# Kernel tuning notes

Measured on AMD Instinct MI355X. Metric: run time of the kernel, lower is better.

## Reference

```python
import jax, jax.numpy as jnp
import numpy as np

U, I, D, NNZ, LAYERS, B = 50000, 50000, 64, 3200000, 3, 4096
N = U + I
L2_REG = 1e-5
EPS = 1e-12


def setup_inputs() -> dict:
    key = jax.random.key(0)
    ks = jax.random.split(key, 12)
    return {
        "users": jax.random.randint(ks[0], (B,), 0, U, dtype=jnp.int64)
        if jax.config.jax_enable_x64 else jax.random.randint(ks[0], (B,), 0, U, dtype=jnp.int32),
        "pos_items": jax.random.randint(ks[1], (B,), 0, N, dtype=jnp.int32),
        "neg_items": jax.random.randint(ks[2], (B,), 0, N, dtype=jnp.int32),
        "rows": jax.random.randint(ks[3], (NNZ,), 0, N, dtype=jnp.int32),
        "cols": jax.random.randint(ks[4], (NNZ,), 0, N, dtype=jnp.int32),
        "vals": jax.random.uniform(ks[5], (NNZ,), dtype=jnp.float32),
        "user_embed": jax.random.normal(ks[6], (U, D), dtype=jnp.float32),
        "item_embed": jax.random.normal(ks[7], (I, D), dtype=jnp.float32),
        "W1": jax.random.normal(ks[8], (LAYERS, D, D), dtype=jnp.float32) * 0.1,
        "b1": jax.random.normal(ks[9], (LAYERS, 1, D), dtype=jnp.float32) * 0.1,
        "W2": jax.random.normal(ks[10], (LAYERS, D, D), dtype=jnp.float32) * 0.1,
        "b2": jax.random.normal(ks[11], (LAYERS, 1, D), dtype=jnp.float32) * 0.1,
    }


def reference(users, pos_items, neg_items, rows, cols, vals,
              user_embed, item_embed, W1, b1, W2, b2):
    # E: [N, D] concatenated user/item embeddings
    E = jnp.concatenate([user_embed, item_embed], axis=0)
    embs = [E]
    for l in range(W1.shape[0]):
        # SpMM: L @ E via edge-wise gather + scatter-add (memory-bound)
        msgs = vals[:, None] * E[cols]                     # [nnz, D]
        L_mul = jax.ops.segment_sum(msgs, rows, num_segments=N)
        A_mul = L_mul + E                                  # A = L + I
        left = A_mul @ W1[l] + b1[l]
        right = (L_mul * E) @ W2[l] + b2[l]
        E = jax.nn.leaky_relu(left + right, negative_slope=0.2)
        # message dropout rate = 0 -> identity
        norm = jnp.maximum(jnp.linalg.norm(E, axis=1, keepdims=True), EPS)
        embs.append(E / norm)
    all_e = jnp.concatenate(embs, axis=1)                  # [N, D*(LAYERS+1)]
    u = all_e[users]
    p = all_e[pos_items]
    n = all_e[neg_items]
    pos_rating = jnp.sum(u * p, axis=1)
    neg_rating = jnp.sum(u * n, axis=1)
    bpr_loss = -jnp.mean(jax.nn.log_sigmoid(pos_rating - neg_rating))
    # faithful to source: neg term is ||n|| (not squared)
    l2norm = (jnp.sum(u ** 2) + jnp.sum(p ** 2) + jnp.sqrt(jnp.sum(n ** 2))) / 2.0
    l2reg = L2_REG * l2norm / u.shape[0]
    return bpr_loss + l2reg
```

## Files before the change

kernel.cpp:

```cpp
#include <hip/hip_runtime.h>
#include <hip/hip_bf16.h>
#include <math.h>

#define U_CNT 50000
#define I_CNT 50000
#define N_CNT 100000
#define D 64
#define NNZ_CNT 3200000
#define LAYERS 3
#define BATCH 4096
#define L2_REG_F 1e-5f
#define EPS_F 1e-12f

#define NBUCKET 391
#define SC_NBLK 256
#define SC_CHUNK 12500
#define BCNT_N (NBUCKET * SC_NBLK)
#define BCNT_NBLK ((BCNT_N + 255) / 256)

typedef __attribute__((ext_vector_type(8))) short short8;
typedef __attribute__((ext_vector_type(4))) float floatx4;

__device__ __forceinline__ unsigned short f32_to_bf16(float f) {
    unsigned int u = __float_as_uint(f);
    u += 0x7FFFu + ((u >> 16) & 1u);
    return (unsigned short)(u >> 16);
}
__device__ __forceinline__ float bf16_to_f32(unsigned short h) {
    return __uint_as_float(((unsigned int)h) << 16);
}
__device__ __forceinline__ float bf16_lo(unsigned int u) {
    return __uint_as_float(u << 16);
}
__device__ __forceinline__ float bf16_hi(unsigned int u) {
    return __uint_as_float(u & 0xFFFF0000u);
}
__device__ __forceinline__ unsigned int pack_bf16(float a, float b) {
    return (unsigned int)f32_to_bf16(a) | ((unsigned int)f32_to_bf16(b) << 16);
}

__global__ void init_E(const float* __restrict__ ue, const float* __restrict__ ie,
                       unsigned short* __restrict__ Ebf, float* __restrict__ all_e) {
    int tid = blockIdx.x * blockDim.x + threadIdx.x;
    if (tid >= N_CNT * D) return;
    int row = tid >> 6;
    int d = tid & 63;
    float v = (row < U_CNT) ? ue[tid] : ie[tid - U_CNT * D];
    Ebf[tid] = f32_to_bf16(v);
    all_e[(size_t)row * 256 + d] = v;
}

__global__ void scan_p1(const int* __restrict__ in, int* __restrict__ bsums, int n) {
    __shared__ int s[256];
    int t = threadIdx.x;
    int i = blockIdx.x * 256 + t;
    int v = (i < n) ? in[i] : 0;
    s[t] = v;
    __syncthreads();
    for (int off = 128; off >= 1; off >>= 1) {
        if (t < off) s[t] += s[t + off];
        __syncthreads();
    }
    if (t == 0) bsums[blockIdx.x] = s[0];
}

__global__ void scan_p2(int* __restrict__ bsums, int nblk) {
    __shared__ int s[512];
    int t = threadIdx.x;
    int v = (t < nblk) ? bsums[t] : 0;
    s[t] = v;
    __syncthreads();
    for (int off = 1; off < 512; off <<= 1) {
        int x = (t >= off) ? s[t - off] : 0;
        __syncthreads();
        s[t] += x;
        __syncthreads();
    }
    if (t < nblk) bsums[t] = s[t] - v;
}

__global__ void scan_p3(const int* __restrict__ in, const int* __restrict__ bsums,
                        int* __restrict__ out, int n) {
    __shared__ int s[256];
    int t = threadIdx.x;
    int i = blockIdx.x * 256 + t;
    int v = (i < n) ? in[i] : 0;
    s[t] = v;
    __syncthreads();
    for (int off = 1; off < 256; off <<= 1) {
        int x = (t >= off) ? s[t - off] : 0;
        __syncthreads();
        s[t] += x;
        __syncthreads();
    }
    if (i < n) out[i] = s[t] - v + bsums[blockIdx.x];
}

__global__ __launch_bounds__(1024) void bucket_hist(const int* __restrict__ rows,
                                                    int* __restrict__ bcnt) {
    __shared__ int h[NBUCKET];
    int blk = blockIdx.x, t = threadIdx.x;
    if (t < NBUCKET) h[t] = 0;
    __syncthreads();
    int s = blk * SC_CHUNK, e = s + SC_CHUNK;
    for (int i = s + t; i < e; i += 1024) atomicAdd(&h[rows[i] >> 8], 1);
    __syncthreads();
    if (t < NBUCKET) bcnt[t * SC_NBLK + blk] = h[t];
}

__global__ __launch_bounds__(1024) void block_scatter(const int* __restrict__ rows,
                                                      const int* __restrict__ cols,
                                                      const float* __restrict__ vals,
                                                      const int* __restrict__ boff,
                                                      float2* __restrict__ bbuf) {
    __shared__ int cur[NBUCKET];
    int blk = blockIdx.x, t = threadIdx.x;
    if (t < NBUCKET) cur[t] = boff[t * SC_NBLK + blk];
    __syncthreads();
    int s = blk * SC_CHUNK, e = s + SC_CHUNK;
    for (int i = s + t; i < e; i += 1024) {
        int r = rows[i];
        int b = r >> 8;
        int p = atomicAdd(&cur[b], 1);
        unsigned int bits = ((unsigned int)(r & 255) << 17) | (unsigned int)cols[i];
        bbuf[p] = make_float2(vals[i], __uint_as_float(bits));
    }
}

__global__ __launch_bounds__(1024) void csr_finalize(const float2* __restrict__ bbuf,
                                                     const int* __restrict__ boff,
                                                     int* __restrict__ row_ptr,
                                                     float2* __restrict__ packed) {
    __shared__ int h[256];
    __shared__ int cur[256];
    int b = blockIdx.x, t = threadIdx.x;
    int s = boff[b * SC_NBLK];
    int e = (b == NBUCKET - 1) ? NNZ_CNT : boff[(b + 1) * SC_NBLK];
    if (t < 256) h[t] = 0;
    __syncthreads();
    for (int i = s + t; i < e; i += 1024)
        atomicAdd(&h[__float_as_uint(bbuf[i].y) >> 17], 1);
    __syncthreads();
    int v = (t < 256) ? h[t] : 0;
    for (int off = 1; off < 256; off <<= 1) {
        int x = (t >= off && t < 256) ? h[t - off] : 0;
        __syncthreads();
        if (t < 256) h[t] += x;
        __syncthreads();
    }
    if (t < 256) {
        int start = s + h[t] - v;
        int row = (b << 8) + t;
        if (row < N_CNT) row_ptr[row] = start;
        cur[t] = start;
        if (b == 0 && t == 0) row_ptr[N_CNT] = NNZ_CNT;
    }
    __syncthreads();
    for (int i = s + t; i < e; i += 1024) {
        float2 rec = bbuf[i];
        unsigned int bits = __float_as_uint(rec.y);
        int p = atomicAdd(&cur[bits >> 17], 1);
        packed[p] = make_float2(rec.x, __int_as_float(bits & 0x1FFFFu));
    }
}

__global__ __launch_bounds__(256) void spmm_bf16(const float2* __restrict__ packed,
                                                 const int* __restrict__ row_ptr,
                                                 const unsigned short* __restrict__ Ebf,
                                                 unsigned short* __restrict__ Lm) {
    int wid = (blockIdx.x * blockDim.x + threadIdx.x) >> 6;
    int lane = threadIdx.x & 63;
    if (wid >= N_CNT) return;
    int s = row_ptr[wid];
    int e = row_ptr[wid + 1];
    int sub = lane >> 2;
    int sl = lane & 3;
    int eidx = sub >> 1;
    int half = sub & 1;
    int dbase = half * 32 + sl * 8;
    float a0 = 0.f, a1 = 0.f, a2 = 0.f, a3 = 0.f;
    float a4 = 0.f, a5 = 0.f, a6 = 0.f, a7 = 0.f;
    int i = s + eidx;
    float2 rec = (i < e) ? packed[i] : make_float2(0.f, __int_as_float(0));
    while (i < e) {
        int inext = i + 8;
        float2 rnext = (inext < e) ? packed[inext] : make_float2(0.f, __int_as_float(0));
        int c = __float_as_int(rec.y);
        uint4 ev = *(const uint4*)(Ebf + (size_t)c * D + dbase);
        float v = rec.x;
        a0 += v * bf16_lo(ev.x); a1 += v * bf16_hi(ev.x);
        a2 += v * bf16_lo(ev.y); a3 += v * bf16_hi(ev.y);
        a4 += v * bf16_lo(ev.z); a5 += v * bf16_hi(ev.z);
        a6 += v * bf16_lo(ev.w); a7 += v * bf16_hi(ev.w);
        rec = rnext;
        i = inext;
    }
#pragma unroll
    for (int off = 32; off >= 8; off >>= 1) {
        a0 += __shfl_xor(a0, off, 64); a1 += __shfl_xor(a1, off, 64);
        a2 += __shfl_xor(a2, off, 64); a3 += __shfl_xor(a3, off, 64);
        a4 += __shfl_xor(a4, off, 64); a5 += __shfl_xor(a5, off, 64);
        a6 += __shfl_xor(a6, off, 64); a7 += __shfl_xor(a7, off, 64);
    }
    if (eidx == 0) {
        unsigned int* dst = (unsigned int*)(Lm + (size_t)wid * D + dbase);
        *(uint4*)dst = make_uint4(pack_bf16(a0, a1), pack_bf16(a2, a3),
                                  pack_bf16(a4, a5), pack_bf16(a6, a7));
    }
}

#define AP 136
__global__ __launch_bounds__(256) void layer_fused_mfma(const unsigned short* __restrict__ Lm,
                                                        unsigned short* __restrict__ Ebf,
                                                        const float* __restrict__ W1,
                                                        const float* __restrict__ b1,
                                                        const float* __restrict__ W2,
                                                        const float* __restrict__ b2,
                                                        float* __restrict__ all_e, int layer) {
    __shared__ unsigned short sBt[64 * AP];
    __shared__ float sBias[64];
    __shared__ unsigned short sA[4][16 * AP];

    int t = threadIdx.x;
    for (int i = t; i < 4096; i += 256) {
        int k = i >> 6, n = i & 63;
        sBt[n * AP + k] = f32_to_bf16(W1[i]);
        sBt[n * AP + 64 + k] = f32_to_bf16(W2[i]);
    }
    if (t < 64) sBias[t] = b1[t] + b2[t];
    __syncthreads();

    int w = t >> 6, lane = t & 63;
    int quad = lane >> 4, l16 = lane & 15;

    short8 bfrag[4][4];
#pragma unroll
    for (int ks = 0; ks < 4; ks++)
#pragma unroll
        for (int ct = 0; ct < 4; ct++)
            bfrag[ks][ct] = *(const short8*)&sBt[(ct * 16 + l16) * AP + ks * 32 + quad * 8];

    float bias[4];
#pragma unroll
    for (int ct = 0; ct < 4; ct++) bias[ct] = sBias[ct * 16 + l16];

    unsigned short* A = sA[w];
    int col_off = (layer + 1) * 64;
    int nwaves = gridDim.x * 4;

    for (int tile = blockIdx.x * 4 + w; tile < N_CNT / 16; tile += nwaves) {
        int rbase = tile * 16;
#pragma unroll
        for (int p = 0; p < 4; p++) {
            int r = p * 4 + quad;
            int c = l16 * 4;
            uint2 lw = *(const uint2*)(Lm + (size_t)(rbase + r) * 64 + c);
            float l0 = bf16_lo(lw.x), l1 = bf16_hi(lw.x);
            float l2 = bf16_lo(lw.y), l3 = bf16_hi(lw.y);
            ushort4 eh = *(const ushort4*)(Ebf + (size_t)(rbase + r) * 64 + c);
            float e0 = bf16_to_f32(eh.x), e1 = bf16_to_f32(eh.y);
            float e2 = bf16_to_f32(eh.z), e3 = bf16_to_f32(eh.w);
            *(uint2*)&A[r * AP + c] = make_uint2(pack_bf16(l0 + e0, l1 + e1),
                                                pack_bf16(l2 + e2, l3 + e3));
            *(uint2*)&A[r * AP + 64 + c] = make_uint2(pack_bf16(l0 * e0, l1 * e1),
                                                      pack_bf16(l2 * e2, l3 * e3));
        }
        floatx4 acc[4];
#pragma unroll
        for (int ct = 0; ct < 4; ct++) {
            acc[ct][0] = bias[ct]; acc[ct][1] = bias[ct];
            acc[ct][2] = bias[ct]; acc[ct][3] = bias[ct];
        }
#pragma unroll
        for (int ks = 0; ks < 4; ks++) {
            short8 af = *(const short8*)&A[l16 * AP + ks * 32 + quad * 8];
#pragma unroll
            for (int ct = 0; ct < 4; ct++)
                acc[ct] = __builtin_amdgcn_mfma_f32_16x16x32_bf16(af, bfrag[ks][ct], acc[ct], 0, 0, 0);
        }
        float y[4][4];
        float ssq[4] = {0.f, 0.f, 0.f, 0.f};
#pragma unroll
        for (int ct = 0; ct < 4; ct++)
#pragma unroll
            for (int reg = 0; reg < 4; reg++) {
                float v = acc[ct][reg];
                v = (v > 0.f) ? v : 0.2f * v;
                y[ct][reg] = v;
                ssq[reg] += v * v;
            }
#pragma unroll
        for (int reg = 0; reg < 4; reg++) {
            float ss = ssq[reg];
            ss += __shfl_xor(ss, 1, 64);
            ss += __shfl_xor(ss, 2, 64);
            ss += __shfl_xor(ss, 4, 64);
            ss += __shfl_xor(ss, 8, 64);
            ssq[reg] = fmaxf(sqrtf(ss), EPS_F);
        }
#pragma unroll
        for (int reg = 0; reg < 4; reg++) {
            int row = rbase + quad * 4 + reg;
            float inv = 1.0f / ssq[reg];
#pragma unroll
            for (int ct = 0; ct < 4; ct++) {
                int col = ct * 16 + l16;
                float v = y[ct][reg];
                Ebf[(size_t)row * 64 + col] = f32_to_bf16(v);
                all_e[(size_t)row * 256 + col_off + col] = v * inv;
            }
        }
    }
}

__device__ __forceinline__ float dot4(float4 a, float4 b) {
    return a.x * b.x + a.y * b.y + a.z * b.z + a.w * b.w;
}

__global__ __launch_bounds__(256) void score_kernel(const float* __restrict__ all_e,
                                                    const int* __restrict__ users,
                                                    const int* __restrict__ pos,
                                                    const int* __restrict__ neg,
                                                    float4* __restrict__ partials) {
    int wid = (blockIdx.x * blockDim.x + threadIdx.x) >> 6;
    int lane = threadIdx.x & 63;
    if (wid >= BATCH) return;
    int ui = users[wid];
    int pi = pos[wid];
    int ni = neg[wid];
    const float4* uv4 = (const float4*)(all_e + (size_t)ui * 256);
    const float4* pv4 = (const float4*)(all_e + (size_t)pi * 256);
    const float4* nv4 = (const float4*)(all_e + (size_t)ni * 256);
    float4 uv = uv4[lane];
    float4 pv = pv4[lane];
    float4 nv = nv4[lane];
    float s_up = dot4(uv, pv);
    float s_un = dot4(uv, nv);
    float s_uu = dot4(uv, uv);
    float s_pp = dot4(pv, pv);
    float s_nn = dot4(nv, nv);
#pragma unroll
    for (int off = 32; off >= 1; off >>= 1) {
        s_up += __shfl_xor(s_up, off, 64);
        s_un += __shfl_xor(s_un, off, 64);
        s_uu += __shfl_xor(s_uu, off, 64);
        s_pp += __shfl_xor(s_pp, off, 64);
        s_nn += __shfl_xor(s_nn, off, 64);
    }
    if (lane == 0) {
        float x = s_up - s_un;
        float ls = fminf(x, 0.f) - log1pf(expf(-fabsf(x)));
        partials[wid] = make_float4(-ls, s_uu, s_pp, s_nn);
    }
}

__global__ __launch_bounds__(256) void reduce_finalize(const float4* __restrict__ partials,
                                                       float* __restrict__ out) {
    __shared__ float4 s[256];
    int t = threadIdx.x;
    float4 a = make_float4(0.f, 0.f, 0.f, 0.f);
    for (int i = t; i < BATCH; i += 256) {
        float4 p = partials[i];
        a.x += p.x; a.y += p.y; a.z += p.z; a.w += p.w;
    }
    s[t] = a;
    __syncthreads();
    for (int off = 128; off >= 1; off >>= 1) {
        if (t < off) {
            s[t].x += s[t + off].x;
            s[t].y += s[t + off].y;
            s[t].z += s[t + off].z;
            s[t].w += s[t + off].w;
        }
        __syncthreads();
    }
    if (t == 0) {
        float bpr = s[0].x / (float)BATCH;
        float l2norm = (s[0].y + s[0].z + sqrtf(s[0].w)) * 0.5f;
        out[0] = bpr + L2_REG_F * l2norm / (float)BATCH;
    }
}

extern "C" void kernel_launch(void* const* d_in, const int* in_sizes, int n_in,
                              void* d_out, int out_size, void* d_ws, size_t ws_size,
                              hipStream_t stream) {
    const int* users = (const int*)d_in[0];
    const int* pos_items = (const int*)d_in[1];
    const int* neg_items = (const int*)d_in[2];
    const int* rows = (const int*)d_in[3];
    const int* cols = (const int*)d_in[4];
    const float* vals = (const float*)d_in[5];
    const float* user_embed = (const float*)d_in[6];
    const float* item_embed = (const float*)d_in[7];
    const float* W1 = (const float*)d_in[8];
    const float* b1 = (const float*)d_in[9];
    const float* W2 = (const float*)d_in[10];
    const float* b2 = (const float*)d_in[11];
    float* out = (float*)d_out;

    char* ws = (char*)d_ws;
    size_t off_alle = 0;
    size_t off_packed = off_alle + (size_t)N_CNT * 256 * 4;
    size_t off_Ebf = off_packed + (size_t)NNZ_CNT * 8;
    size_t off_Lm = off_Ebf + (size_t)N_CNT * D * 2;
    size_t off_rowptr = off_Lm + (size_t)N_CNT * D * 2;
    size_t off_blkB = off_rowptr + 400128;
    size_t off_bcnt = off_blkB + 2048;
    size_t off_part = off_bcnt + 400384;

    float* all_e = (float*)(ws + off_alle);
    float2* bbuf = (float2*)(ws + off_alle);
    float2* packed = (float2*)(ws + off_packed);
    unsigned short* Ebf = (unsigned short*)(ws + off_Ebf);
    unsigned short* Lm = (unsigned short*)(ws + off_Lm);
    int* row_ptr = (int*)(ws + off_rowptr);
    int* blkB = (int*)(ws + off_blkB);
    int* bcnt = (int*)(ws + off_bcnt);
    float4* partials = (float4*)(ws + off_part);

    bucket_hist<<<SC_NBLK, 1024, 0, stream>>>(rows, bcnt);
    scan_p1<<<BCNT_NBLK, 256, 0, stream>>>(bcnt, blkB, BCNT_N);
    scan_p2<<<1, 512, 0, stream>>>(blkB, BCNT_NBLK);
    scan_p3<<<BCNT_NBLK, 256, 0, stream>>>(bcnt, blkB, bcnt, BCNT_N);
    block_scatter<<<SC_NBLK, 1024, 0, stream>>>(rows, cols, vals, bcnt, bbuf);
    csr_finalize<<<NBUCKET, 1024, 0, stream>>>(bbuf, bcnt, row_ptr, packed);

    init_E<<<(N_CNT * D) / 256, 256, 0, stream>>>(user_embed, item_embed, Ebf, all_e);

    for (int l = 0; l < LAYERS; l++) {
        spmm_bf16<<<(N_CNT * 64) / 256, 256, 0, stream>>>(packed, row_ptr, Ebf, Lm);
        layer_fused_mfma<<<784, 256, 0, stream>>>(Lm, Ebf, W1 + (size_t)l * 4096,
                                                  b1 + (size_t)l * 64, W2 + (size_t)l * 4096,
                                                  b2 + (size_t)l * 64, all_e, l);
    }

    score_kernel<<<(BATCH * 64) / 256, 256, 0, stream>>>(all_e, users, pos_items, neg_items,
                                                         partials);
    reduce_finalize<<<1, 256, 0, stream>>>(partials, out);
}
```

Before: 440.2 us.

## Gather FP8 per-row-scaled embeddings and 15-bit packed edge values in SpMM

Keeps an FP8 e4m3 copy of the embedding table with per-row absmax scales, written in init and at the end of each layer's fused MFMA kernel. The SpMM then gathers 8 bytes per lane instead of 16 bytes of bf16. Edge records are compressed from 8 to 4 bytes by quantizing vals to 15 bits next to the 17-bit column index. This halves the random-gather and edge-stream traffic of the memory-bound SpMM, at the cost of much lower precision in the message sums. It also adds an extra scale load per edge and extra quantization work in the layer kernel.

Measured after the change: 460.7 us. 4.7% more time.

```diff
diff --git a/kernel.cpp b/kernel.cpp
--- a/kernel.cpp
+++ b/kernel.cpp
@@ -1,5 +1,6 @@
 #include <hip/hip_runtime.h>
 #include <hip/hip_bf16.h>
+#include <hip/hip_fp8.h>
 #include <math.h>
 
 #define U_CNT 50000
@@ -20,6 +21,7 @@
 
 typedef __attribute__((ext_vector_type(8))) short short8;
 typedef __attribute__((ext_vector_type(4))) float floatx4;
+typedef __attribute__((ext_vector_type(2))) float f32x2v;
 
 __device__ __forceinline__ unsigned short f32_to_bf16(float f) {
     unsigned int u = __float_as_uint(f);
@@ -39,15 +41,50 @@
     return (unsigned int)f32_to_bf16(a) | ((unsigned int)f32_to_bf16(b) << 16);
 }
 
-__global__ void init_E(const float* __restrict__ ue, const float* __restrict__ ie,
-                       unsigned short* __restrict__ Ebf, float* __restrict__ all_e) {
-    int tid = blockIdx.x * blockDim.x + threadIdx.x;
-    if (tid >= N_CNT * D) return;
-    int row = tid >> 6;
-    int d = tid & 63;
-    float v = (row < U_CNT) ? ue[tid] : ie[tid - U_CNT * D];
-    Ebf[tid] = f32_to_bf16(v);
-    all_e[(size_t)row * 256 + d] = v;
+__device__ __forceinline__ unsigned char f32_to_fp8(float v) {
+#if __has_builtin(__builtin_amdgcn_cvt_pk_fp8_f32)
+    return (unsigned char)(__builtin_amdgcn_cvt_pk_fp8_f32(v, 0.0f, 0, false) & 0xFF);
+#else
+    __hip_fp8_e4m3 t(v);
+    return (unsigned char)t.__x;
+#endif
+}
+template <bool HI>
+__device__ __forceinline__ f32x2v fp8x2_to_f32(unsigned int w) {
+#if __has_builtin(__builtin_amdgcn_cvt_pk_f32_fp8)
+    return __builtin_amdgcn_cvt_pk_f32_fp8((int)w, HI);
+#else
+    unsigned int s = HI ? (w >> 16) : (w & 0xFFFFu);
+    __hip_fp8_e4m3 a, b;
+    a.__x = (unsigned char)(s & 0xFF);
+    b.__x = (unsigned char)((s >> 8) & 0xFF);
+    f32x2v r;
+    r.x = (float)a;
+    r.y = (float)b;
+    return r;
+#endif
+}
+
+__global__ __launch_bounds__(256) void init_E(const float* __restrict__ ue,
+                                              const float* __restrict__ ie,
+                                              unsigned short* __restrict__ Ebf,
+                                              unsigned char* __restrict__ Efp8,
+                                              float* __restrict__ scales,
+                                              float* __restrict__ all_e) {
+    int wid = (blockIdx.x * blockDim.x + threadIdx.x) >> 6;
+    int lane = threadIdx.x & 63;
+    if (wid >= N_CNT) return;
+    size_t base = (size_t)wid * 64;
+    float v = (wid < U_CNT) ? ue[base + lane] : ie[base - (size_t)U_CNT * 64 + lane];
+    Ebf[base + lane] = f32_to_bf16(v);
+    all_e[(size_t)wid * 256 + lane] = v;
+    float m = fabsf(v);
+#pragma unroll
+    for (int off = 32; off >= 1; off >>= 1) m = fmaxf(m, __shfl_xor(m, off, 64));
+    m = fmaxf(m, 1e-30f);
+    float esc = 224.0f / m;
+    Efp8[base + lane] = f32_to_fp8(v * esc);
+    if (lane == 0) scales[wid] = m * (1.0f / 224.0f);
 }
 
 __global__ void scan_p1(const int* __restrict__ in, int* __restrict__ bsums, int n) {
@@ -130,7 +167,7 @@
 __global__ __launch_bounds__(1024) void csr_finalize(const float2* __restrict__ bbuf,
                                                      const int* __restrict__ boff,
                                                      int* __restrict__ row_ptr,
-                                                     float2* __restrict__ packed) {
+                                                     unsigned int* __restrict__ packed) {
     __shared__ int h[256];
     __shared__ int cur[256];
     int b = blockIdx.x, t = threadIdx.x;
@@ -160,39 +197,43 @@
         float2 rec = bbuf[i];
         unsigned int bits = __float_as_uint(rec.y);
         int p = atomicAdd(&cur[bits >> 17], 1);
-        packed[p] = make_float2(rec.x, __int_as_float(bits & 0x1FFFFu));
-    }
-}
-
-__global__ __launch_bounds__(256) void spmm_bf16(const float2* __restrict__ packed,
-                                                 const int* __restrict__ row_ptr,
-                                                 const unsigned short* __restrict__ Ebf,
-                                                 unsigned short* __restrict__ Lm) {
+        unsigned int q = (unsigned int)(rec.x * 32767.0f + 0.5f);
+        packed[p] = (q << 17) | (bits & 0x1FFFFu);
+    }
+}
+
+__global__ __launch_bounds__(256) void spmm_fp8(const unsigned int* __restrict__ packed,
+                                                const int* __restrict__ row_ptr,
+                                                const unsigned char* __restrict__ Efp8,
+                                                const float* __restrict__ scales,
+                                                unsigned short* __restrict__ Lm) {
     int wid = (blockIdx.x * blockDim.x + threadIdx.x) >> 6;
     int lane = threadIdx.x & 63;
     if (wid >= N_CNT) return;
     int s = row_ptr[wid];
     int e = row_ptr[wid + 1];
-    int sub = lane >> 2;
-    int sl = lane & 3;
-    int eidx = sub >> 1;
-    int half = sub & 1;
-    int dbase = half * 32 + sl * 8;
+    int eidx = lane >> 3;
+    int dlane = lane & 7;
     float a0 = 0.f, a1 = 0.f, a2 = 0.f, a3 = 0.f;
     float a4 = 0.f, a5 = 0.f, a6 = 0.f, a7 = 0.f;
     int i = s + eidx;
-    float2 rec = (i < e) ? packed[i] : make_float2(0.f, __int_as_float(0));
+    unsigned int u = (i < e) ? packed[i] : 0u;
     while (i < e) {
         int inext = i + 8;
-        float2 rnext = (inext < e) ? packed[inext] : make_float2(0.f, __int_as_float(0));
-        int c = __float_as_int(rec.y);
-        uint4 ev = *(const uint4*)(Ebf + (size_t)c * D + dbase);
-        float v = rec.x;
-        a0 += v * bf16_lo(ev.x); a1 += v * bf16_hi(ev.x);
-        a2 += v * bf16_lo(ev.y); a3 += v * bf16_hi(ev.y);
-        a4 += v * bf16_lo(ev.z); a5 += v * bf16_hi(ev.z);
-        a6 += v * bf16_lo(ev.w); a7 += v * bf16_hi(ev.w);
-        rec = rnext;
+        unsigned int un = (inext < e) ? packed[inext] : 0u;
+        int c = (int)(u & 0x1FFFFu);
+        float sc = scales[c];
+        uint2 g = *(const uint2*)(Efp8 + ((size_t)c << 6) + (dlane << 3));
+        float vs = (float)(u >> 17) * (1.0f / 32767.0f) * sc;
+        f32x2v p0 = fp8x2_to_f32<false>(g.x);
+        f32x2v p1 = fp8x2_to_f32<true>(g.x);
+        f32x2v p2 = fp8x2_to_f32<false>(g.y);
+        f32x2v p3 = fp8x2_to_f32<true>(g.y);
+        a0 += vs * p0.x; a1 += vs * p0.y;
+        a2 += vs * p1.x; a3 += vs * p1.y;
+        a4 += vs * p2.x; a5 += vs * p2.y;
+        a6 += vs * p3.x; a7 += vs * p3.y;
+        u = un;
         i = inext;
     }
 #pragma unroll
@@ -203,7 +244,7 @@
         a6 += __shfl_xor(a6, off, 64); a7 += __shfl_xor(a7, off, 64);
     }
     if (eidx == 0) {
-        unsigned int* dst = (unsigned int*)(Lm + (size_t)wid * D + dbase);
+        unsigned int* dst = (unsigned int*)(Lm + (size_t)wid * D + dlane * 8);
         *(uint4*)dst = make_uint4(pack_bf16(a0, a1), pack_bf16(a2, a3),
                                   pack_bf16(a4, a5), pack_bf16(a6, a7));
     }
@@ -212,6 +253,8 @@
 #define AP 136
 __global__ __launch_bounds__(256) void layer_fused_mfma(const unsigned short* __restrict__ Lm,
                                                         unsigned short* __restrict__ Ebf,
+                                                        unsigned char* __restrict__ Efp8,
+                                                        float* __restrict__ scales,
                                                         const float* __restrict__ W1,
                                                         const float* __restrict__ b1,
                                                         const float* __restrict__ W2,
@@ -280,6 +323,7 @@
         }
         float y[4][4];
         float ssq[4] = {0.f, 0.f, 0.f, 0.f};
+        float rmx[4] = {0.f, 0.f, 0.f, 0.f};
 #pragma unroll
         for (int ct = 0; ct < 4; ct++)
 #pragma unroll
@@ -288,6 +332,7 @@
                 v = (v > 0.f) ? v : 0.2f * v;
                 y[ct][reg] = v;
                 ssq[reg] += v * v;
+                rmx[reg] = fmaxf(rmx[reg], fabsf(v));
             }
 #pragma unroll
         for (int reg = 0; reg < 4; reg++) {
@@ -297,6 +342,12 @@
             ss += __shfl_xor(ss, 4, 64);
             ss += __shfl_xor(ss, 8, 64);
             ssq[reg] = fmaxf(sqrtf(ss), EPS_F);
+            float mm = rmx[reg];
+            mm = fmaxf(mm, __shfl_xor(mm, 1, 64));
+            mm = fmaxf(mm, __shfl_xor(mm, 2, 64));
+            mm = fmaxf(mm, __shfl_xor(mm, 4, 64));
+            mm = fmaxf(mm, __shfl_xor(mm, 8, 64));
+            rmx[reg] = fmaxf(mm, 1e-30f);
         }
 #pragma unroll
         for (int reg = 0; reg < 4; reg++) {
@@ -309,6 +360,25 @@
                 Ebf[(size_t)row * 64 + col] = f32_to_bf16(v);
                 all_e[(size_t)row * 256 + col_off + col] = v * inv;
             }
+        }
+        if (layer < 2) {
+            unsigned char* sb = (unsigned char*)A;
+#pragma unroll
+            for (int reg = 0; reg < 4; reg++) {
+                float esc = 224.0f / rmx[reg];
+                int rl = quad * 4 + reg;
+#pragma unroll
+                for (int ct = 0; ct < 4; ct++)
+                    sb[rl * 64 + ct * 16 + l16] = f32_to_fp8(y[ct][reg] * esc);
+            }
+            if (l16 == 0) {
+#pragma unroll
+                for (int reg = 0; reg < 4; reg++)
+                    scales[rbase + quad * 4 + reg] = rmx[reg] * (1.0f / 224.0f);
+            }
+            __builtin_amdgcn_wave_barrier();
+            uint4 ov = *(const uint4*)(sb + lane * 16);
+            *(uint4*)(Efp8 + (size_t)rbase * 64 + lane * 16) = ov;
         }
     }
 }
@@ -401,8 +471,10 @@
     char* ws = (char*)d_ws;
     size_t off_alle = 0;
     size_t off_packed = off_alle + (size_t)N_CNT * 256 * 4;
-    size_t off_Ebf = off_packed + (size_t)NNZ_CNT * 8;
-    size_t off_Lm = off_Ebf + (size_t)N_CNT * D * 2;
+    size_t off_Ebf = off_packed + (size_t)NNZ_CNT * 4;
+    size_t off_Efp8 = off_Ebf + (size_t)N_CNT * D * 2;
+    size_t off_scales = off_Efp8 + (size_t)N_CNT * D;
+    size_t off_Lm = off_scales + (size_t)N_CNT * 4;
     size_t off_rowptr = off_Lm + (size_t)N_CNT * D * 2;
     size_t off_blkB = off_rowptr + 400128;
     size_t off_bcnt = off_blkB + 2048;
@@ -410,8 +482,10 @@
 
     float* all_e = (float*)(ws + off_alle);
     float2* bbuf = (float2*)(ws + off_alle);
-    float2* packed = (float2*)(ws + off_packed);
+    unsigned int* packed = (unsigned int*)(ws + off_packed);
     unsigned short* Ebf = (unsigned short*)(ws + off_Ebf);
+    unsigned char* Efp8 = (unsigned char*)(ws + off_Efp8);
+    float* scales = (float*)(ws + off_scales);
     unsigned short* Lm = (unsigned short*)(ws + off_Lm);
     int* row_ptr = (int*)(ws + off_rowptr);
     int* blkB = (int*)(ws + off_blkB);
@@ -425,13 +499,15 @@
     block_scatter<<<SC_NBLK, 1024, 0, stream>>>(rows, cols, vals, bcnt, bbuf);
     csr_finalize<<<NBUCKET, 1024, 0, stream>>>(bbuf, bcnt, row_ptr, packed);
 
-    init_E<<<(N_CNT * D) / 256, 256, 0, stream>>>(user_embed, item_embed, Ebf, all_e);
+    init_E<<<(N_CNT * 64) / 256, 256, 0, stream>>>(user_embed, item_embed, Ebf, Efp8,
+                                                   scales, all_e);
 
     for (int l = 0; l < LAYERS; l++) {
-        spmm_bf16<<<(N_CNT * 64) / 256, 256, 0, stream>>>(packed, row_ptr, Ebf, Lm);
-        layer_fused_mfma<<<784, 256, 0, stream>>>(Lm, Ebf, W1 + (size_t)l * 4096,
-                                                  b1 + (size_t)l * 64, W2 + (size_t)l * 4096,
-                                                  b2 + (size_t)l * 64, all_e, l);
+        spmm_fp8<<<(N_CNT * 64) / 256, 256, 0, stream>>>(packed, row_ptr, Efp8, scales, Lm);
+        layer_fused_mfma<<<784, 256, 0, stream>>>(Lm, Ebf, Efp8, scales,
+                                                  W1 + (size_t)l * 4096, b1 + (size_t)l * 64,
+                                                  W2 + (size_t)l * 4096, b2 + (size_t)l * 64,
+                                                  all_e, l);
     }
 
     score_kernel<<<(BATCH * 64) / 256, 256, 0, stream>>>(all_e, users, pos_items, neg_items,
```
